# Kernel optimization log

Hardware: AMD Instinct MI355X
Metric: run time of the kernel (lower is better)

The kernel has to match this reference:

```python
import jax, jax.numpy as jnp
import numpy as np

THRESHOLD = 1.0
SLOPE = 25.0

@jax.custom_vjp
def spike(m):
    # Heaviside forward
    return (m >= THRESHOLD).astype(m.dtype)

def _spike_fwd(m):
    return spike(m), m

def _spike_bwd(m, g):
    # fast-sigmoid surrogate gradient: 1 / (1 + slope*|m - thr|)^2
    base = 1.0 + SLOPE * jnp.abs(m - THRESHOLD)
    return (g / (base * base),)

spike.defvjp(_spike_fwd, _spike_bwd)

def setup_inputs() -> dict:
    key = jax.random.key(0)
    k1, k2 = jax.random.split(key)
    T, B, D = 64, 256, 2048
    currents = jax.random.normal(k1, (T, B, D), dtype=jnp.float32)
    # beta_raw initialized like torch: log(beta/(1-beta)) with beta=0.9, plus
    # tiny noise to make it a realistic learned parameter
    raw = float(np.log(0.9 / 0.1))
    beta_raw = jnp.full((D,), raw, dtype=jnp.float32) + 0.01 * jax.random.normal(k2, (D,), dtype=jnp.float32)
    return {"currents": currents, "beta_raw": beta_raw}

def reference(currents, beta_raw):
    beta = jax.nn.sigmoid(beta_raw)  # (dim,), broadcasts over (B, dim)

    def step(mem, cur):
        mem = beta * mem + cur
        s = spike(mem)
        mem = mem * (1.0 - jax.lax.stop_gradient(s))  # reset, detached
        return mem, s

    mem0 = jnp.zeros_like(currents[0])
    final_mem, all_spikes = jax.lax.scan(step, mem0, currents)
    return all_spikes, final_mem
```

## Files before the change

### kernel.cpp

```cpp
#include <hip/hip_runtime.h>


#define T_STEPS 64
#define B_SZ 256
#define D_SZ 2048
#define BD (B_SZ * D_SZ)
#define NVEC (BD / 4)

__global__ __launch_bounds__(256) void lif_fwd_kernel(
    const float* __restrict__ currents,
    const float* __restrict__ beta_raw,
    float* __restrict__ out)
{
    const int idx = blockIdx.x * blockDim.x + threadIdx.x;
    const int d4  = idx & (D_SZ / 4 - 1);

    const float4 br = reinterpret_cast<const float4*>(beta_raw)[d4];
    const float b0 = (float)(1.0 / (1.0 + exp(-(double)br.x)));
    const float b1 = (float)(1.0 / (1.0 + exp(-(double)br.y)));
    const float b2 = (float)(1.0 / (1.0 + exp(-(double)br.z)));
    const float b3 = (float)(1.0 / (1.0 + exp(-(double)br.w)));

    const float4* __restrict__ cur = reinterpret_cast<const float4*>(currents) + idx;
    float4* __restrict__ spk       = reinterpret_cast<float4*>(out) + idx;

    float m0 = 0.f, m1 = 0.f, m2 = 0.f, m3 = 0.f;

    #pragma unroll 8
    for (int t = 0; t < T_STEPS; ++t) {
        const float4 c = cur[t * NVEC];
        m0 = __fadd_rn(__fmul_rn(b0, m0), c.x);
        m1 = __fadd_rn(__fmul_rn(b1, m1), c.y);
        m2 = __fadd_rn(__fmul_rn(b2, m2), c.z);
        m3 = __fadd_rn(__fmul_rn(b3, m3), c.w);

        const float s0 = (m0 >= 1.0f) ? 1.0f : 0.0f;
        const float s1 = (m1 >= 1.0f) ? 1.0f : 0.0f;
        const float s2 = (m2 >= 1.0f) ? 1.0f : 0.0f;
        const float s3 = (m3 >= 1.0f) ? 1.0f : 0.0f;

        spk[t * NVEC] = make_float4(s0, s1, s2, s3);

        m0 = (s0 != 0.f) ? 0.f : m0;
        m1 = (s1 != 0.f) ? 0.f : m1;
        m2 = (s2 != 0.f) ? 0.f : m2;
        m3 = (s3 != 0.f) ? 0.f : m3;
    }

    reinterpret_cast<float4*>(out + (size_t)T_STEPS * BD)[idx] =
        make_float4(m0, m1, m2, m3);
}

extern "C" void kernel_launch(void* const* d_in, const int* in_sizes, int n_in,
                              void* d_out, int out_size, void* d_ws, size_t ws_size,
                              hipStream_t stream)
{
    const float* currents = (const float*)d_in[0];
    const float* beta_raw = (const float*)d_in[1];
    float* out = (float*)d_out;

    const int threads = 256;
    const int blocks  = NVEC / threads;
    lif_fwd_kernel<<<blocks, threads, 0, stream>>>(currents, beta_raw, out);
}
```

Before: 233.4 us.

## Use float2 per thread with 8-deep register prefetch of currents

Each thread now handles two neurons instead of four, which doubles the thread count and raises parallelism. Currents for the next 8 timesteps are held in a rotating register buffer so that loads are issued well before they are used. The aim is to hide memory latency in this bandwidth-bound scan. In exchange, the kernel uses narrower 8-byte accesses and more registers per element in flight.

```diff
diff --git a/kernel.cpp b/kernel.cpp
--- a/kernel.cpp
+++ b/kernel.cpp
@@ -5,7 +5,8 @@
 #define B_SZ 256
 #define D_SZ 2048
 #define BD (B_SZ * D_SZ)
-#define NVEC (BD / 4)
+#define NVEC2 (BD / 2)
+#define PF 8
 
 __global__ __launch_bounds__(256) void lif_fwd_kernel(
     const float* __restrict__ currents,
@@ -13,42 +14,42 @@
     float* __restrict__ out)
 {
     const int idx = blockIdx.x * blockDim.x + threadIdx.x;
-    const int d4  = idx & (D_SZ / 4 - 1);
+    const int d2  = idx & (D_SZ / 2 - 1);
 
-    const float4 br = reinterpret_cast<const float4*>(beta_raw)[d4];
+    const float2 br = reinterpret_cast<const float2*>(beta_raw)[d2];
     const float b0 = (float)(1.0 / (1.0 + exp(-(double)br.x)));
     const float b1 = (float)(1.0 / (1.0 + exp(-(double)br.y)));
-    const float b2 = (float)(1.0 / (1.0 + exp(-(double)br.z)));
-    const float b3 = (float)(1.0 / (1.0 + exp(-(double)br.w)));
 
-    const float4* __restrict__ cur = reinterpret_cast<const float4*>(currents) + idx;
-    float4* __restrict__ spk       = reinterpret_cast<float4*>(out) + idx;
+    const float2* __restrict__ cur = reinterpret_cast<const float2*>(currents) + idx;
+    float2* __restrict__ spk       = reinterpret_cast<float2*>(out) + idx;
 
-    float m0 = 0.f, m1 = 0.f, m2 = 0.f, m3 = 0.f;
+    float m0 = 0.f, m1 = 0.f;
 
-    #pragma unroll 8
+    float2 buf[PF];
+    #pragma unroll
+    for (int k = 0; k < PF; ++k)
+        buf[k] = cur[k * NVEC2];
+
+    #pragma unroll
     for (int t = 0; t < T_STEPS; ++t) {
-        const float4 c = cur[t * NVEC];
+        const float2 c = buf[t & (PF - 1)];
+        if (t + PF < T_STEPS)
+            buf[t & (PF - 1)] = cur[(t + PF) * NVEC2];
+
         m0 = __fadd_rn(__fmul_rn(b0, m0), c.x);
         m1 = __fadd_rn(__fmul_rn(b1, m1), c.y);
-        m2 = __fadd_rn(__fmul_rn(b2, m2), c.z);
-        m3 = __fadd_rn(__fmul_rn(b3, m3), c.w);
 
         const float s0 = (m0 >= 1.0f) ? 1.0f : 0.0f;
         const float s1 = (m1 >= 1.0f) ? 1.0f : 0.0f;
-        const float s2 = (m2 >= 1.0f) ? 1.0f : 0.0f;
-        const float s3 = (m3 >= 1.0f) ? 1.0f : 0.0f;
 
-        spk[t * NVEC] = make_float4(s0, s1, s2, s3);
+        spk[t * NVEC2] = make_float2(s0, s1);
 
         m0 = (s0 != 0.f) ? 0.f : m0;
         m1 = (s1 != 0.f) ? 0.f : m1;
-        m2 = (s2 != 0.f) ? 0.f : m2;
-        m3 = (s3 != 0.f) ? 0.f : m3;
     }
 
-    reinterpret_cast<float4*>(out + (size_t)T_STEPS * BD)[idx] =
-        make_float4(m0, m1, m2, m3);
+    reinterpret_cast<float2*>(out + (size_t)T_STEPS * BD)[idx] =
+        make_float2(m0, m1);
 }
 
 extern "C" void kernel_launch(void* const* d_in, const int* in_sizes, int n_in,
@@ -60,6 +61,6 @@
     float* out = (float*)d_out;
 
     const int threads = 256;
-    const int blocks  = NVEC / threads;
+    const int blocks  = NVEC2 / threads;
     lif_fwd_kernel<<<blocks, threads, 0, stream>>>(currents, beta_raw, out);
 }
```

Result: no change. 230.2 us (-1.4%).
